# Kernel optimization log

Hardware: AMD Instinct MI355X
Metric: run time of the kernel (lower is better)

Reference implementation:

```python
import jax, jax.numpy as jnp
import numpy as np

T = 100.0  # temperature, from init_kwargs
B = 4096
D = 128
NUM_CLASSES = 10


def setup_inputs() -> dict:
    key = jax.random.key(0)
    kx, ky = jax.random.split(key)
    x = jax.random.normal(kx, (B, D), dtype=jnp.float32)
    y = jax.random.randint(ky, (B,), 0, NUM_CLASSES, dtype=jnp.int64)
    return {"x": x, "y": y}


def reference(x, y):
    # Pairwise squared Euclidean distances: dist[i,j] = ||x_i - x_j||^2
    sq = jnp.sum(x * x, axis=1)                      # [b]
    dist = sq[:, None] + sq[None, :] - 2.0 * (x @ x.T)  # [b, b]
    dist = jnp.maximum(dist, 0.0)                    # clamp fp error; diag -> 0

    e = jnp.exp(-dist / T)                           # [b, b]; e[i,i] = 1

    b = x.shape[0]
    same = (y[:, None] == y[None, :])                # same-label mask
    not_self = ~jnp.eye(b, dtype=bool)

    # numerator: sum over j != i with y[j] == y[i]
    num = jnp.sum(jnp.where(same & not_self, e, 0.0), axis=1)  # [b]
    # denominator: sum over ALL j, including j == i (exp(0) = 1), as in the
    # original loop where the denominator accumulates unconditionally
    den = jnp.sum(e, axis=1)                         # [b]

    return jnp.mean(-jnp.log(num / den))
```

## Files before the change

### kernel.cpp

```cpp
#include <hip/hip_runtime.h>
#include <hip/hip_bf16.h>

#define NB 4096
#define NTB 32

typedef short v8s __attribute__((ext_vector_type(8)));
typedef float v4f __attribute__((ext_vector_type(4)));


__global__ __launch_bounds__(256) void prep_kernel(const float* __restrict__ x,
        float* __restrict__ sq, float* __restrict__ out,
        unsigned short* __restrict__ xb) {
    int tid = threadIdx.x;
    int row = blockIdx.x * 8 + (tid >> 5);
    int lane = tid & 31;
    const float4* xg = (const float4*)x;
    float4 v = xg[row * 32 + lane];
    __hip_bfloat16 h0 = __float2bfloat16(v.x), h1 = __float2bfloat16(v.y);
    __hip_bfloat16 h2 = __float2bfloat16(v.z), h3 = __float2bfloat16(v.w);
    ushort4 u4;
    u4.x = *(unsigned short*)&h0; u4.y = *(unsigned short*)&h1;
    u4.z = *(unsigned short*)&h2; u4.w = *(unsigned short*)&h3;
    ((ushort4*)xb)[row * 32 + lane] = u4;
    float s = v.x * v.x + v.y * v.y + v.z * v.z + v.w * v.w;
    #pragma unroll
    for (int off = 16; off > 0; off >>= 1) s += __shfl_down(s, off);
    if (lane == 0) sq[row] = s;
    if (blockIdx.x == 0 && tid == 0) out[0] = 0.f;
}

__global__ __launch_bounds__(256) void snn_sym(const unsigned short* __restrict__ xb,
        const int* __restrict__ y, const float* __restrict__ sqg,
        float2* __restrict__ P) {
    __shared__ float part[2][128][34];
    __shared__ float2 part2[2][128];
    __shared__ float sqi[128], sqj[128];
    __shared__ int yi[128], yj[128];

    const int tid = threadIdx.x;
    const int wave = tid >> 6;
    const int lane = tid & 63;
    const int wm = wave >> 1;
    const int wn = wave & 1;
    const int lr = lane & 15;
    const int q  = lane >> 4;

    int t = blockIdx.x, bi = 0, rem = NTB;
    while (t >= rem) { t -= rem; ++bi; --rem; }
    const int bj = bi + t;
    const int i0 = bi * 128, j0 = bj * 128;

    if (tid < 128) {
        sqi[tid] = sqg[i0 + tid]; sqj[tid] = sqg[j0 + tid];
        yi[tid] = y[i0 + tid];    yj[tid] = y[j0 + tid];
    }

    const v8s* xg = (const v8s*)xb;
    const v8s* arow = xg + (i0 + wm * 64 + lr) * 16 + q;
    const v8s* brow = xg + (j0 + wn * 64 + lr) * 16 + q;

    v4f acc[4][4];
    #pragma unroll
    for (int mt = 0; mt < 4; ++mt)
        #pragma unroll
        for (int nt = 0; nt < 4; ++nt)
            acc[mt][nt] = (v4f){0.f, 0.f, 0.f, 0.f};

    #pragma unroll
    for (int kk = 0; kk < 4; ++kk) {
        v8s af[4], bf[4];
        #pragma unroll
        for (int mt = 0; mt < 4; ++mt) af[mt] = arow[mt * 256 + kk * 4];
        #pragma unroll
        for (int nt = 0; nt < 4; ++nt) bf[nt] = brow[nt * 256 + kk * 4];
        #pragma unroll
        for (int mt = 0; mt < 4; ++mt)
            #pragma unroll
            for (int nt = 0; nt < 4; ++nt)
                acc[mt][nt] = __builtin_amdgcn_mfma_f32_16x16x32_bf16(
                    af[mt], bf[nt], acc[mt][nt], 0, 0, 0);
    }

    __syncthreads();

    float sqj_r[4]; int yj_r[4], jgl[4];
    #pragma unroll
    for (int nt = 0; nt < 4; ++nt) {
        int jc = wn * 64 + nt * 16 + lr;
        sqj_r[nt] = sqj[jc]; yj_r[nt] = yj[jc]; jgl[nt] = j0 + jc;
    }
    float cn[4] = {0.f, 0.f, 0.f, 0.f}, cd[4] = {0.f, 0.f, 0.f, 0.f};
    #pragma unroll
    for (int mt = 0; mt < 4; ++mt) {
        #pragma unroll
        for (int r = 0; r < 4; ++r) {
            int rloc = wm * 64 + mt * 16 + q * 4 + r;
            float si = sqi[rloc]; int yir = yi[rloc]; int ig = i0 + rloc;
            float n = 0.f, d = 0.f;
            #pragma unroll
            for (int nt = 0; nt < 4; ++nt) {
                float dist = fmaxf(si + sqj_r[nt] - 2.f * acc[mt][nt][r], 0.f);
                float e = __builtin_amdgcn_exp2f(dist * -0.014426950408889634f);
                d += e;
                float me = (yir == yj_r[nt] && ig != jgl[nt]) ? e : 0.f;
                n += me;
                cd[nt] += e; cn[nt] += me;
            }
            *(float2*)&part[wn][rloc][lr * 2] = make_float2(n, d);
        }
    }
    #pragma unroll
    for (int nt = 0; nt < 4; ++nt) {
        float n2 = cn[nt] + __shfl_xor(cn[nt], 16); n2 += __shfl_xor(n2, 32);
        float d2 = cd[nt] + __shfl_xor(cd[nt], 16); d2 += __shfl_xor(d2, 32);
        if (q == 0) part2[wm][wn * 64 + nt * 16 + lr] = make_float2(n2, d2);
    }
    __syncthreads();

    {
        int row = tid >> 1, h = tid & 1;
        const float2* p = (const float2*)&part[h][row][0];
        float sn = 0.f, sd = 0.f;
        #pragma unroll
        for (int c = 0; c < 16; ++c) { float2 v = p[c]; sn += v.x; sd += v.y; }
        sn += __shfl_down(sn, 1); sd += __shfl_down(sd, 1);
        if (h == 0) P[(bi * NTB + bj) * 128 + row] = make_float2(sn, sd);
    }
    if (bi != bj && tid < 128) {
        float2 a = part2[0][tid], b = part2[1][tid];
        P[(bj * NTB + bi) * 128 + tid] = make_float2(a.x + b.x, a.y + b.y);
    }
}

__global__ __launch_bounds__(256) void snn_final(const float2* __restrict__ P,
        float* __restrict__ out) {
    __shared__ float wsum[4];
    int i = blockIdx.x * 256 + threadIdx.x;
    int ib = i >> 7, il = i & 127;
    float n = 0.f, d = 0.f;
    #pragma unroll
    for (int s = 0; s < NTB; ++s) {
        float2 v = P[(ib * NTB + s) * 128 + il];
        n += v.x; d += v.y;
    }
    float l = -__logf(n / d);
    #pragma unroll
    for (int off = 32; off > 0; off >>= 1) l += __shfl_down(l, off);
    if ((threadIdx.x & 63) == 0) wsum[threadIdx.x >> 6] = l;
    __syncthreads();
    if (threadIdx.x == 0)
        atomicAdd(out, (wsum[0] + wsum[1] + wsum[2] + wsum[3]) * (1.0f / NB));
}

extern "C" void kernel_launch(void* const* d_in, const int* in_sizes, int n_in,
                              void* d_out, int out_size, void* d_ws, size_t ws_size,
                              hipStream_t stream) {
    const float* x = (const float*)d_in[0];
    const int*   y = (const int*)d_in[1];
    float* out = (float*)d_out;
    float* sq  = (float*)d_ws;
    unsigned short* xb = (unsigned short*)(sq + NB);
    float2* P = (float2*)(xb + NB * 128);

    prep_kernel<<<NB / 8, 256, 0, stream>>>(x, sq, out, xb);
    snn_sym<<<NTB * (NTB + 1) / 2, 256, 0, stream>>>(xb, y, sq, P);
    snn_final<<<NB / 256, 256, 0, stream>>>(P, out);
}
```

Before: 77.38 us.

## Switch to per-wave 32x32 symmetric tiles without shared memory

```diff
diff --git a/kernel.cpp b/kernel.cpp
--- a/kernel.cpp
+++ b/kernel.cpp
@@ -2,7 +2,8 @@
 #include <hip/hip_bf16.h>
 
 #define NB 4096
-#define NTB 32
+#define NT 128
+#define NTILES (NT * (NT + 1) / 2)
 
 typedef short v8s __attribute__((ext_vector_type(8)));
 typedef float v4f __attribute__((ext_vector_type(4)));
@@ -29,118 +30,133 @@
     if (blockIdx.x == 0 && tid == 0) out[0] = 0.f;
 }
 
-__global__ __launch_bounds__(256) void snn_sym(const unsigned short* __restrict__ xb,
+__global__ __launch_bounds__(256) void snn_wave(const unsigned short* __restrict__ xb,
         const int* __restrict__ y, const float* __restrict__ sqg,
-        float2* __restrict__ P) {
-    __shared__ float part[2][128][34];
-    __shared__ float2 part2[2][128];
-    __shared__ float sqi[128], sqj[128];
-    __shared__ int yi[128], yj[128];
+        float2* __restrict__ Q) {
+    const int tid = threadIdx.x;
+    const int wid = tid >> 6;
+    const int lane = tid & 63;
+    const int lr = lane & 15;
+    const int q = lane >> 4;
 
-    const int tid = threadIdx.x;
-    const int wave = tid >> 6;
-    const int lane = tid & 63;
-    const int wm = wave >> 1;
-    const int wn = wave & 1;
-    const int lr = lane & 15;
-    const int q  = lane >> 4;
+    int t = blockIdx.x * 4 + wid;
 
-    int t = blockIdx.x, bi = 0, rem = NTB;
-    while (t >= rem) { t -= rem; ++bi; --rem; }
-    const int bj = bi + t;
-    const int i0 = bi * 128, j0 = bj * 128;
+    float sf = sqrtf((float)(66049 - 8 * t));
+    int bi = (int)((257.0f - sf) * 0.5f);
+    int st = 128 * bi - ((bi * (bi - 1)) >> 1);
+    while (t < st) { --bi; st = 128 * bi - ((bi * (bi - 1)) >> 1); }
+    while (t >= st + (NT - bi)) { st += NT - bi; ++bi; }
+    const int bj = bi + (t - st);
+    const int i0 = bi * 32, j0 = bj * 32;
+    const bool diag = (bi == bj);
 
-    if (tid < 128) {
-        sqi[tid] = sqg[i0 + tid]; sqj[tid] = sqg[j0 + tid];
-        yi[tid] = y[i0 + tid];    yj[tid] = y[j0 + tid];
+    float sqi_l = 0.f, sqj_l = 0.f; int yi_l = 0, yj_l = 0;
+    if (lane < 32) {
+        sqi_l = sqg[i0 + lane]; yi_l = y[i0 + lane];
+        sqj_l = sqg[j0 + lane]; yj_l = y[j0 + lane];
     }
 
     const v8s* xg = (const v8s*)xb;
-    const v8s* arow = xg + (i0 + wm * 64 + lr) * 16 + q;
-    const v8s* brow = xg + (j0 + wn * 64 + lr) * 16 + q;
+    const v8s* arow = xg + (i0 + lr) * 16 + q;
+    const v8s* brow = xg + (j0 + lr) * 16 + q;
+    v4f acc[2][2];
+    #pragma unroll
+    for (int mt = 0; mt < 2; ++mt)
+        #pragma unroll
+        for (int nt = 0; nt < 2; ++nt)
+            acc[mt][nt] = (v4f){0.f, 0.f, 0.f, 0.f};
+    #pragma unroll
+    for (int kk = 0; kk < 4; ++kk) {
+        v8s a0 = arow[kk * 4];
+        v8s a1 = arow[256 + kk * 4];
+        v8s b0 = brow[kk * 4];
+        v8s b1 = brow[256 + kk * 4];
+        acc[0][0] = __builtin_amdgcn_mfma_f32_16x16x32_bf16(a0, b0, acc[0][0], 0, 0, 0);
+        acc[0][1] = __builtin_amdgcn_mfma_f32_16x16x32_bf16(a0, b1, acc[0][1], 0, 0, 0);
+        acc[1][0] = __builtin_amdgcn_mfma_f32_16x16x32_bf16(a1, b0, acc[1][0], 0, 0, 0);
+        acc[1][1] = __builtin_amdgcn_mfma_f32_16x16x32_bf16(a1, b1, acc[1][1], 0, 0, 0);
+    }
 
-    v4f acc[4][4];
+    float si[2][4]; int yir[2][4];
     #pragma unroll
-    for (int mt = 0; mt < 4; ++mt)
+    for (int mt = 0; mt < 2; ++mt)
         #pragma unroll
-        for (int nt = 0; nt < 4; ++nt)
-            acc[mt][nt] = (v4f){0.f, 0.f, 0.f, 0.f};
+        for (int r = 0; r < 4; ++r) {
+            int rl = mt * 16 + q * 4 + r;
+            si[mt][r] = __shfl(sqi_l, rl);
+            yir[mt][r] = __shfl(yi_l, rl);
+        }
+    float sj[2]; int yjc[2];
+    #pragma unroll
+    for (int nt = 0; nt < 2; ++nt) {
+        int cl = nt * 16 + lr;
+        sj[nt] = __shfl(sqj_l, cl);
+        yjc[nt] = __shfl(yj_l, cl);
+    }
+
+    float rn[2][4], rd[2][4];
+    float cn[2] = {0.f, 0.f}, cd[2] = {0.f, 0.f};
+    #pragma unroll
+    for (int mt = 0; mt < 2; ++mt) {
+        #pragma unroll
+        for (int r = 0; r < 4; ++r) {
+            int ig = i0 + mt * 16 + q * 4 + r;
+            float n = 0.f, d = 0.f;
+            #pragma unroll
+            for (int nt = 0; nt < 2; ++nt) {
+                float dist = fmaxf(si[mt][r] + sj[nt] - 2.f * acc[mt][nt][r], 0.f);
+                float e = __builtin_amdgcn_exp2f(dist * -0.014426950408889634f);
+                bool ok = (yir[mt][r] == yjc[nt]) && (ig != (j0 + nt * 16 + lr));
+                float me = ok ? e : 0.f;
+                d += e; n += me;
+                cd[nt] += e; cn[nt] += me;
+            }
+            rn[mt][r] = n; rd[mt][r] = d;
+        }
+    }
 
     #pragma unroll
-    for (int kk = 0; kk < 4; ++kk) {
-        v8s af[4], bf[4];
+    for (int mt = 0; mt < 2; ++mt)
         #pragma unroll
-        for (int mt = 0; mt < 4; ++mt) af[mt] = arow[mt * 256 + kk * 4];
+        for (int r = 0; r < 4; ++r)
+            #pragma unroll
+            for (int off = 1; off < 16; off <<= 1) {
+                rn[mt][r] += __shfl_xor(rn[mt][r], off);
+                rd[mt][r] += __shfl_xor(rd[mt][r], off);
+            }
+    #pragma unroll
+    for (int nt = 0; nt < 2; ++nt)
         #pragma unroll
-        for (int nt = 0; nt < 4; ++nt) bf[nt] = brow[nt * 256 + kk * 4];
+        for (int off = 16; off < 64; off <<= 1) {
+            cn[nt] += __shfl_xor(cn[nt], off);
+            cd[nt] += __shfl_xor(cd[nt], off);
+        }
+
+    float2* Qrow = Q + (bi * NT + bj) * 32;
+    if (lr == 0) {
         #pragma unroll
-        for (int mt = 0; mt < 4; ++mt)
+        for (int mt = 0; mt < 2; ++mt)
             #pragma unroll
-            for (int nt = 0; nt < 4; ++nt)
-                acc[mt][nt] = __builtin_amdgcn_mfma_f32_16x16x32_bf16(
-                    af[mt], bf[nt], acc[mt][nt], 0, 0, 0);
+            for (int r = 0; r < 4; ++r)
+                Qrow[mt * 16 + q * 4 + r] = make_float2(rn[mt][r], rd[mt][r]);
     }
-
-    __syncthreads();
-
-    float sqj_r[4]; int yj_r[4], jgl[4];
-    #pragma unroll
-    for (int nt = 0; nt < 4; ++nt) {
-        int jc = wn * 64 + nt * 16 + lr;
-        sqj_r[nt] = sqj[jc]; yj_r[nt] = yj[jc]; jgl[nt] = j0 + jc;
-    }
-    float cn[4] = {0.f, 0.f, 0.f, 0.f}, cd[4] = {0.f, 0.f, 0.f, 0.f};
-    #pragma unroll
-    for (int mt = 0; mt < 4; ++mt) {
+    if (!diag && q == 0) {
+        float2* Qcol = Q + (bj * NT + bi) * 32;
         #pragma unroll
-        for (int r = 0; r < 4; ++r) {
-            int rloc = wm * 64 + mt * 16 + q * 4 + r;
-            float si = sqi[rloc]; int yir = yi[rloc]; int ig = i0 + rloc;
-            float n = 0.f, d = 0.f;
-            #pragma unroll
-            for (int nt = 0; nt < 4; ++nt) {
-                float dist = fmaxf(si + sqj_r[nt] - 2.f * acc[mt][nt][r], 0.f);
-                float e = __builtin_amdgcn_exp2f(dist * -0.014426950408889634f);
-                d += e;
-                float me = (yir == yj_r[nt] && ig != jgl[nt]) ? e : 0.f;
-                n += me;
-                cd[nt] += e; cn[nt] += me;
-            }
-            *(float2*)&part[wn][rloc][lr * 2] = make_float2(n, d);
-        }
-    }
-    #pragma unroll
-    for (int nt = 0; nt < 4; ++nt) {
-        float n2 = cn[nt] + __shfl_xor(cn[nt], 16); n2 += __shfl_xor(n2, 32);
-        float d2 = cd[nt] + __shfl_xor(cd[nt], 16); d2 += __shfl_xor(d2, 32);
-        if (q == 0) part2[wm][wn * 64 + nt * 16 + lr] = make_float2(n2, d2);
-    }
-    __syncthreads();
-
-    {
-        int row = tid >> 1, h = tid & 1;
-        const float2* p = (const float2*)&part[h][row][0];
-        float sn = 0.f, sd = 0.f;
-        #pragma unroll
-        for (int c = 0; c < 16; ++c) { float2 v = p[c]; sn += v.x; sd += v.y; }
-        sn += __shfl_down(sn, 1); sd += __shfl_down(sd, 1);
-        if (h == 0) P[(bi * NTB + bj) * 128 + row] = make_float2(sn, sd);
-    }
-    if (bi != bj && tid < 128) {
-        float2 a = part2[0][tid], b = part2[1][tid];
-        P[(bj * NTB + bi) * 128 + tid] = make_float2(a.x + b.x, a.y + b.y);
+        for (int nt = 0; nt < 2; ++nt)
+            Qcol[nt * 16 + lr] = make_float2(cn[nt], cd[nt]);
     }
 }
 
-__global__ __launch_bounds__(256) void snn_final(const float2* __restrict__ P,
+__global__ __launch_bounds__(256) void snn_final(const float2* __restrict__ Q,
         float* __restrict__ out) {
     __shared__ float wsum[4];
     int i = blockIdx.x * 256 + threadIdx.x;
-    int ib = i >> 7, il = i & 127;
+    int bi = i >> 5, il = i & 31;
     float n = 0.f, d = 0.f;
-    #pragma unroll
-    for (int s = 0; s < NTB; ++s) {
-        float2 v = P[(ib * NTB + s) * 128 + il];
+    #pragma unroll 8
+    for (int b = 0; b < NT; ++b) {
+        float2 v = Q[(bi * NT + b) * 32 + il];
         n += v.x; d += v.y;
     }
     float l = -__logf(n / d);
@@ -160,9 +176,9 @@
     float* out = (float*)d_out;
     float* sq  = (float*)d_ws;
     unsigned short* xb = (unsigned short*)(sq + NB);
-    float2* P = (float2*)(xb + NB * 128);
+    float2* Q = (float2*)(xb + NB * 128);
 
     prep_kernel<<<NB / 8, 256, 0, stream>>>(x, sq, out, xb);
-    snn_sym<<<NTB * (NTB + 1) / 2, 256, 0, stream>>>(xb, y, sq, P);
-    snn_final<<<NB / 256, 256, 0, stream>>>(P, out);
+    snn_wave<<<NTILES / 4, 256, 0, stream>>>(xb, y, sq, Q);
+    snn_final<<<NB / 256, 256, 0, stream>>>(Q, out);
 }
```

Measured after the change: 85.99 us. 11.1% more time.
